# Optimization experiments

Hardware: AMD Instinct MI355X
Metric: run time of the kernel (lower is better)

## Reference

```python
import jax, jax.numpy as jnp
import numpy as np


def setup_inputs() -> dict:
    key = jax.random.key(0)
    kq, kk, kv = jax.random.split(key, 3)
    bs, K, t, d, vocab = 32, 16, 4, 64, 8192
    q = jax.random.normal(kq, (bs, K, t, d), dtype=jnp.float32)
    k = jax.random.normal(kk, (bs, vocab, t, d), dtype=jnp.float32)
    v = jax.random.normal(kv, (bs, vocab, t, d), dtype=jnp.float32)
    return {"q": q, "k": k, "v": v}


def reference(q, k, v):
    # q: (bs,K,t,d), k/v: (bs,vocab,t,d)
    scale = q.shape[-1] ** -0.5
    # logits/attn: (bs,t,K,vocab) -- matches torch transpose(1,2) then matmul
    logits = jnp.einsum('bktd,bvtd->btkv', q * scale, k)
    attn = jax.nn.softmax(logits, axis=-1)
    # per-row argmax over vocab for every t (vectorized over the t loop)
    tokens = jnp.swapaxes(jnp.argmax(attn, axis=-1), 1, 2)  # (bs,K,t)
    # weighted sum over vocab, back to (bs,K,t,d)
    out = jnp.einsum('btkv,bvtd->bktd', attn, v)
    return (out, tokens)
```

## Files before the change

### kernel.cpp

```cpp
#include <hip/hip_runtime.h>
#include <math.h>


#define BSZ 32
#define KQ  16
#define TT  4
#define DD  64
#define VOC 8192
#define TR  16
#define NW  4
#define PART 1088
#define FIXM 20.0f

typedef float v2f __attribute__((ext_vector_type(2)));

#define BR4(k) ((((k)&1)<<3)|(((k)&2)<<1)|(((k)&4)>>1)|(((k)&8)>>3))

__device__ __forceinline__ float fxor1(float x) {
    return __int_as_float(__builtin_amdgcn_update_dpp(
        0, __float_as_int(x), 0xB1 , 0xF, 0xF, true));
}
__device__ __forceinline__ float fxor2(float x) {
    return __int_as_float(__builtin_amdgcn_update_dpp(
        0, __float_as_int(x), 0x4E , 0xF, 0xF, true));
}
__device__ __forceinline__ float fxor8(float x) {
    return __int_as_float(__builtin_amdgcn_update_dpp(
        0, __float_as_int(x), 0x128 , 0xF, 0xF, true));
}
#define XSWZ4(x) __int_as_float(__builtin_amdgcn_ds_swizzle(__float_as_int(x), 0x101F))

__global__ __launch_bounds__(256, 2)
void bat_main(const float* __restrict__ Q, const float* __restrict__ Kp,
              const float* __restrict__ Vp, float* __restrict__ ws, int NC)
{
    __shared__ __align__(16) float mOs[NW * KQ * 64];
    __shared__ __align__(16) float ps[NW * 64];
    __shared__ float lS[NW * KQ], bvS[NW * KQ], biS[NW * KQ];

    const int tid  = threadIdx.x;
    const int w    = tid >> 6;
    const int lane = tid & 63;
    const int o    = lane & 15;
    const int r    = lane >> 4;
    const int kkq  = BR4(o);
    const int bid  = blockIdx.x;
    const int c    = bid % NC;
    const int t    = (bid / NC) % TT;
    const int b    = bid / (NC * TT);
    const int CHUNK = VOC / NC;
    const int NT    = CHUNK / TR;
    const int row0  = c * CHUNK;

    v2f qp[8][4];
    {
        const float4* qg = reinterpret_cast<const float4*>(Q + (size_t)b * KQ * TT * DD);
#pragma unroll
        for (int p2 = 0; p2 < 8; ++p2) {
            float4 qa = qg[((2 * p2)     * TT + t) * (DD / 4) + o];
            float4 qb = qg[((2 * p2 + 1) * TT + t) * (DD / 4) + o];
            qa.x *= 0.125f; qa.y *= 0.125f; qa.z *= 0.125f; qa.w *= 0.125f;
            qb.x *= 0.125f; qb.y *= 0.125f; qb.z *= 0.125f; qb.w *= 0.125f;
            qp[p2][0] = (v2f){qa.x, qb.x};
            qp[p2][1] = (v2f){qa.y, qb.y};
            qp[p2][2] = (v2f){qa.z, qb.z};
            qp[p2][3] = (v2f){qa.w, qb.w};
        }
    }

    const size_t rstride = TT * DD;
    const float* gKl = Kp + ((size_t)b * VOC + row0 + w * 4 + r) * rstride
                          + (size_t)t * DD + (o << 2);
    const float* gV = Vp + ((size_t)b * VOC + row0 + w * 4) * rstride
                         + (size_t)t * DD + lane;

#define LK(it, kd)                                                          \
    kd = *reinterpret_cast<const float4*>(gKl + (size_t)(it) * TR * rstride);
#define SV(it, d0, d1, d2, d3)                                  \
    {                                                           \
        const float* vbp = gV + (size_t)(it) * TR * rstride;    \
        d0 = vbp[0];                                            \
        d1 = vbp[rstride];                                      \
        d2 = vbp[2 * rstride];                                  \
        d3 = vbp[3 * rstride];                                  \
    }

    v2f O2[8];
#pragma unroll
    for (int i = 0; i < 8; ++i) O2[i] = (v2f){0.f, 0.f};
    float l0 = 0.f, bv0 = -INFINITY;
    int   bi0 = 0;
    float va0, va1, va2, va3, vb0, vb1, vb2, vb3;
    float4 kA, kB;

    auto C = [&](int it, const float4& kx,
                 float v0, float v1, float v2, float v3) {
        const v2f kxx = (v2f){kx.x, kx.x};
        const v2f kxy = (v2f){kx.y, kx.y};
        const v2f kxz = (v2f){kx.z, kx.z};
        const v2f kxw = (v2f){kx.w, kx.w};
        v2f acc2[8];
#pragma unroll
        for (int p2 = 0; p2 < 8; ++p2) {
            v2f s = qp[p2][0] * kxx;
            s = __builtin_elementwise_fma(qp[p2][1], kxy, s);
            s = __builtin_elementwise_fma(qp[p2][2], kxz, s);
            s = __builtin_elementwise_fma(qp[p2][3], kxw, s);
            acc2[p2] = s;
        }
        float acc[KQ];
#pragma unroll
        for (int p2 = 0; p2 < 8; ++p2) { acc[2*p2] = acc2[p2].x; acc[2*p2+1] = acc2[p2].y; }

        float nn[8];
#pragma unroll
        for (int j = 0; j < 8; ++j) {
            const float sA = fxor1(acc[j]);
            const float sB = fxor1(acc[j + 8]);
            nn[j] = (o & 1) ? (acc[j + 8] + sB) : (acc[j] + sA);
        }
        float mm[4];
#pragma unroll
        for (int j = 0; j < 4; ++j) {
            const float sA = fxor2(nn[j]);
            const float sB = fxor2(nn[j + 4]);
            mm[j] = (o & 2) ? (nn[j + 4] + sB) : (nn[j] + sA);
        }
        float p0, p1;
        {
            const float sA = XSWZ4(mm[0]);
            const float sB = XSWZ4(mm[2]);
            const float sC = XSWZ4(mm[1]);
            const float sD = XSWZ4(mm[3]);
            p0 = (o & 4) ? (mm[2] + sB) : (mm[0] + sA);
            p1 = (o & 4) ? (mm[3] + sD) : (mm[1] + sC);
        }
        float f;
        {
            const float sA = fxor8(p0);
            const float sB = fxor8(p1);
            f = (o & 8) ? (p1 + sB) : (p0 + sA);
        }

        const int rowAbs = row0 + it * TR + w * 4 + r;
        if (f > bv0) { bv0 = f; bi0 = rowAbs; }
        const float p = __expf(f - FIXM);
        l0 += p;
        ps[w * 64 + r * 16 + kkq] = p;

#pragma unroll
        for (int rr = 0; rr < 4; ++rr) {
            const float vv = (rr == 0) ? v0 : (rr == 1) ? v1 : (rr == 2) ? v2 : v3;
            const v2f vv2 = (v2f){vv, vv};
            const float* pp = ps + w * 64 + rr * 16;
            const float4 pa = *reinterpret_cast<const float4*>(pp + 0);
            const float4 pb = *reinterpret_cast<const float4*>(pp + 4);
            const float4 pc = *reinterpret_cast<const float4*>(pp + 8);
            const float4 pd = *reinterpret_cast<const float4*>(pp + 12);
            O2[0] = __builtin_elementwise_fma((v2f){pa.x, pa.y}, vv2, O2[0]);
            O2[1] = __builtin_elementwise_fma((v2f){pa.z, pa.w}, vv2, O2[1]);
            O2[2] = __builtin_elementwise_fma((v2f){pb.x, pb.y}, vv2, O2[2]);
            O2[3] = __builtin_elementwise_fma((v2f){pb.z, pb.w}, vv2, O2[3]);
            O2[4] = __builtin_elementwise_fma((v2f){pc.x, pc.y}, vv2, O2[4]);
            O2[5] = __builtin_elementwise_fma((v2f){pc.z, pc.w}, vv2, O2[5]);
            O2[6] = __builtin_elementwise_fma((v2f){pd.x, pd.y}, vv2, O2[6]);
            O2[7] = __builtin_elementwise_fma((v2f){pd.z, pd.w}, vv2, O2[7]);
        }
    };

    LK(0, kA); SV(0, va0, va1, va2, va3);
    LK(1, kB); SV(1, vb0, vb1, vb2, vb3);
    for (int it = 0; it + 2 < NT; it += 2) {
        asm volatile("s_waitcnt vmcnt(5)" ::: "memory");
        __builtin_amdgcn_sched_barrier(0);
        C(it, kA, va0, va1, va2, va3);
        LK(it + 2, kA); SV(it + 2, va0, va1, va2, va3);
        asm volatile("s_waitcnt vmcnt(5)" ::: "memory");
        __builtin_amdgcn_sched_barrier(0);
        C(it + 1, kB, vb0, vb1, vb2, vb3);
        LK(it + 3, kB); SV(it + 3, vb0, vb1, vb2, vb3);
    }
    asm volatile("s_waitcnt vmcnt(5)" ::: "memory");
    __builtin_amdgcn_sched_barrier(0);
    C(NT - 2, kA, va0, va1, va2, va3);
    asm volatile("s_waitcnt vmcnt(0)" ::: "memory");
    __builtin_amdgcn_sched_barrier(0);
    C(NT - 1, kB, vb0, vb1, vb2, vb3);

    l0 += __shfl_xor(l0, 16, 64);
    l0 += __shfl_xor(l0, 32, 64);
#pragma unroll
    for (int s = 16; s <= 32; s <<= 1) {
        const float ov = __shfl_xor(bv0, s, 64);
        const int   oi = __shfl_xor(bi0, s, 64);
        if (ov > bv0 || (ov == bv0 && oi < bi0)) { bv0 = ov; bi0 = oi; }
    }

    float* mO = mOs;
#pragma unroll
    for (int okk = 0; okk < KQ; ++okk)
        mO[(w * KQ + okk) * 64 + lane] = (okk & 1) ? O2[okk >> 1].y : O2[okk >> 1].x;
    if (r == 0) {
        lS[w * KQ + kkq]  = l0;
        bvS[w * KQ + kkq] = bv0;
        biS[w * KQ + kkq] = (float)bi0;
    }
    __syncthreads();

    float* wp = ws + (((size_t)(b * TT + t)) * NC + c) * PART;
    {
        const int mk = tid >> 4, d4 = tid & 15;
        float4 os = make_float4(0.f, 0.f, 0.f, 0.f);
#pragma unroll
        for (int ww = 0; ww < NW; ++ww) {
            const float4 ov = *reinterpret_cast<const float4*>(&mO[(ww * KQ + mk) * 64 + d4 * 4]);
            os.x += ov.x; os.y += ov.y; os.z += ov.z; os.w += ov.w;
        }
        *reinterpret_cast<float4*>(wp + mk * 64 + d4 * 4) = os;
    }
    if (tid < KQ) {
        float L = 0.f;
#pragma unroll
        for (int ww = 0; ww < NW; ++ww) L += lS[ww * KQ + tid];
        float BV = -INFINITY, BI = 0.f;
#pragma unroll
        for (int ww = 0; ww < NW; ++ww) {
            const float v   = bvS[ww * KQ + tid];
            const float ixf = biS[ww * KQ + tid];
            if (v > BV || (v == BV && ixf < BI)) { BV = v; BI = ixf; }
        }
        wp[1024 + tid] = L;
        wp[1040 + tid] = BV;
        wp[1056 + tid] = BI;
    }
}

__global__ __launch_bounds__(256)
void bat_combine(const float* __restrict__ ws, float* __restrict__ out, int NC)
{
    const int bt  = blockIdx.x;
    const int b   = bt >> 2, t = bt & 3;
    const int tid = threadIdx.x;
    const int kk  = tid >> 4;
    const int d4  = tid & 15;
    const float* base = ws + (size_t)bt * NC * PART;

    float4 O = make_float4(0.f, 0.f, 0.f, 0.f);
    float  L = 0.f;
    for (int c = 0; c < NC; ++c) {
        const float* wp = base + (size_t)c * PART;
        const float4 oc = *reinterpret_cast<const float4*>(wp + kk * 64 + d4 * 4);
        O.x += oc.x; O.y += oc.y; O.z += oc.z; O.w += oc.w;
        L   += wp[1024 + kk];
    }
    const float inv = 1.f / L;
    const size_t oidx = (((size_t)b * KQ + kk) * TT + t) * DD + d4 * 4;
    *reinterpret_cast<float4*>(&out[oidx]) =
        make_float4(O.x * inv, O.y * inv, O.z * inv, O.w * inv);

    if (d4 == 0) {
        float BV = -INFINITY, BI = 0.f;
        for (int c = 0; c < NC; ++c) {
            const float* wp = base + (size_t)c * PART;
            const float v   = wp[1040 + kk];
            const float ixf = wp[1056 + kk];
            if (v > BV || (v == BV && ixf < BI)) { BV = v; BI = ixf; }
        }
        out[(size_t)BSZ * KQ * TT * DD + (size_t)(b * KQ + kk) * TT + t] = BI;
    }
}

extern "C" void kernel_launch(void* const* d_in, const int* in_sizes, int n_in,
                              void* d_out, int out_size, void* d_ws, size_t ws_size,
                              hipStream_t stream)
{
    const float* q = (const float*)d_in[0];
    const float* k = (const float*)d_in[1];
    const float* v = (const float*)d_in[2];
    float* out = (float*)d_out;
    float* ws  = (float*)d_ws;

    int NC = 16;
    while (NC > 1 && (size_t)BSZ * TT * NC * PART * sizeof(float) > ws_size) NC >>= 1;

    bat_main<<<dim3(BSZ * TT * NC), dim3(256), 0, stream>>>(q, k, v, ws, NC);
    bat_combine<<<dim3(BSZ * TT), dim3(256), 0, stream>>>(ws, out, NC);
}
```

Before: 134.8 us.

## Software-pipeline QK logits and PV accumulation with double-buffered probabilities

Splits the per-tile body into a logits/softmax stage and a P·V accumulation stage. The PV update for tile i-1 now runs after the logits for tile i, using a double-buffered shared probability array. K and V loads are staggered so V arrives one tile later, and a prologue and epilogue handle the ends. The vocab split count also drops from 16 to 8 chunks, which halves the grid and doubles per-block work. This trades some parallelism for less combine traffic, and the vmcnt waits must stay correct across the new load order.

```diff
diff --git a/kernel.cpp b/kernel.cpp
--- a/kernel.cpp
+++ b/kernel.cpp
@@ -35,7 +35,7 @@
               const float* __restrict__ Vp, float* __restrict__ ws, int NC)
 {
     __shared__ __align__(16) float mOs[NW * KQ * 64];
-    __shared__ __align__(16) float ps[NW * 64];
+    __shared__ __align__(16) float ps2[2 * NW * 64];
     __shared__ float lS[NW * KQ], bvS[NW * KQ], biS[NW * KQ];
 
     const int tid  = threadIdx.x;
@@ -93,8 +93,7 @@
     float va0, va1, va2, va3, vb0, vb1, vb2, vb3;
     float4 kA, kB;
 
-    auto C = [&](int it, const float4& kx,
-                 float v0, float v1, float v2, float v3) {
+    auto CL = [&](int it, const float4& kx) {
         const v2f kxx = (v2f){kx.x, kx.x};
         const v2f kxy = (v2f){kx.y, kx.y};
         const v2f kxz = (v2f){kx.z, kx.z};
@@ -146,21 +145,24 @@
         if (f > bv0) { bv0 = f; bi0 = rowAbs; }
         const float p = __expf(f - FIXM);
         l0 += p;
-        ps[w * 64 + r * 16 + kkq] = p;
-
+        ps2[(it & 1) * (NW * 64) + w * 64 + r * 16 + kkq] = p;
+    };
+
+    auto PV = [&](int pit, float v0, float v1, float v2, float v3) {
+        const float* pb = ps2 + (pit & 1) * (NW * 64) + w * 64;
 #pragma unroll
         for (int rr = 0; rr < 4; ++rr) {
             const float vv = (rr == 0) ? v0 : (rr == 1) ? v1 : (rr == 2) ? v2 : v3;
             const v2f vv2 = (v2f){vv, vv};
-            const float* pp = ps + w * 64 + rr * 16;
+            const float* pp = pb + rr * 16;
             const float4 pa = *reinterpret_cast<const float4*>(pp + 0);
-            const float4 pb = *reinterpret_cast<const float4*>(pp + 4);
+            const float4 pbv = *reinterpret_cast<const float4*>(pp + 4);
             const float4 pc = *reinterpret_cast<const float4*>(pp + 8);
             const float4 pd = *reinterpret_cast<const float4*>(pp + 12);
             O2[0] = __builtin_elementwise_fma((v2f){pa.x, pa.y}, vv2, O2[0]);
             O2[1] = __builtin_elementwise_fma((v2f){pa.z, pa.w}, vv2, O2[1]);
-            O2[2] = __builtin_elementwise_fma((v2f){pb.x, pb.y}, vv2, O2[2]);
-            O2[3] = __builtin_elementwise_fma((v2f){pb.z, pb.w}, vv2, O2[3]);
+            O2[2] = __builtin_elementwise_fma((v2f){pbv.x, pbv.y}, vv2, O2[2]);
+            O2[3] = __builtin_elementwise_fma((v2f){pbv.z, pbv.w}, vv2, O2[3]);
             O2[4] = __builtin_elementwise_fma((v2f){pc.x, pc.y}, vv2, O2[4]);
             O2[5] = __builtin_elementwise_fma((v2f){pc.z, pc.w}, vv2, O2[5]);
             O2[6] = __builtin_elementwise_fma((v2f){pd.x, pd.y}, vv2, O2[6]);
@@ -168,24 +170,41 @@
         }
     };
 
-    LK(0, kA); SV(0, va0, va1, va2, va3);
-    LK(1, kB); SV(1, vb0, vb1, vb2, vb3);
-    for (int it = 0; it + 2 < NT; it += 2) {
+    LK(0, kA); SV(0, va0, va1, va2, va3); LK(1, kB);
+    asm volatile("s_waitcnt vmcnt(5)" ::: "memory");
+    __builtin_amdgcn_sched_barrier(0);
+    CL(0, kA);
+    LK(2, kA); SV(1, vb0, vb1, vb2, vb3);
+
+    for (int it = 1; it + 3 < NT; it += 2) {
         asm volatile("s_waitcnt vmcnt(5)" ::: "memory");
         __builtin_amdgcn_sched_barrier(0);
-        C(it, kA, va0, va1, va2, va3);
-        LK(it + 2, kA); SV(it + 2, va0, va1, va2, va3);
+        CL(it, kB);
+        PV(it - 1, va0, va1, va2, va3);
+        LK(it + 2, kB); SV(it + 1, va0, va1, va2, va3);
         asm volatile("s_waitcnt vmcnt(5)" ::: "memory");
         __builtin_amdgcn_sched_barrier(0);
-        C(it + 1, kB, vb0, vb1, vb2, vb3);
-        LK(it + 3, kB); SV(it + 3, vb0, vb1, vb2, vb3);
+        CL(it + 1, kA);
+        PV(it, vb0, vb1, vb2, vb3);
+        LK(it + 3, kA); SV(it + 2, vb0, vb1, vb2, vb3);
     }
     asm volatile("s_waitcnt vmcnt(5)" ::: "memory");
     __builtin_amdgcn_sched_barrier(0);
-    C(NT - 2, kA, va0, va1, va2, va3);
+    CL(NT - 3, kB);
+    PV(NT - 4, va0, va1, va2, va3);
+    LK(NT - 1, kB); SV(NT - 2, va0, va1, va2, va3);
+    asm volatile("s_waitcnt vmcnt(5)" ::: "memory");
+    __builtin_amdgcn_sched_barrier(0);
+    CL(NT - 2, kA);
+    PV(NT - 3, vb0, vb1, vb2, vb3);
+    SV(NT - 1, vb0, vb1, vb2, vb3);
+    asm volatile("s_waitcnt vmcnt(4)" ::: "memory");
+    __builtin_amdgcn_sched_barrier(0);
+    CL(NT - 1, kB);
+    PV(NT - 2, va0, va1, va2, va3);
     asm volatile("s_waitcnt vmcnt(0)" ::: "memory");
     __builtin_amdgcn_sched_barrier(0);
-    C(NT - 1, kB, vb0, vb1, vb2, vb3);
+    PV(NT - 1, vb0, vb1, vb2, vb3);
 
     l0 += __shfl_xor(l0, 16, 64);
     l0 += __shfl_xor(l0, 32, 64);
@@ -280,7 +299,7 @@
     float* out = (float*)d_out;
     float* ws  = (float*)d_ws;
 
-    int NC = 16;
+    int NC = 8;
     while (NC > 1 && (size_t)BSZ * TT * NC * PART * sizeof(float) > ws_size) NC >>= 1;
 
     bat_main<<<dim3(BSZ * TT * NC), dim3(256), 0, stream>>>(q, k, v, ws, NC);
```

Result: slower. 140.3 us (+4.0%).
